# Kernel tuning notes

Measured on AMD Instinct MI355X. Metric: run time of the kernel, lower is better.

## Reference

```python
import jax, jax.numpy as jnp
import numpy as np

EPS = 1e-12  # F.normalize denominator clamp


def setup_inputs() -> dict:
    key = jax.random.key(0)
    k1, k2, k3, k4 = jax.random.split(key, 4)
    bs, d, nc, ncl, cs, ny = 8192, 768, 64, 500, 100, 1000
    train_embedding = jax.random.normal(k1, (bs, d), dtype=jnp.float32)
    clusters = jax.random.normal(k2, (ncl, cs, d), dtype=jnp.float32)
    # init_concept: uniform in [-0.5, 0.5]
    concept = jax.random.uniform(k3, (d, nc), dtype=jnp.float32, minval=-0.5, maxval=0.5)
    W_h = jax.random.normal(k4, (d, ny), dtype=jnp.float32) * 0.02
    b_h = jnp.zeros((ny,), dtype=jnp.float32)
    return {"train_embedding": train_embedding, "clusters": clusters,
            "concept": concept, "W_h": W_h, "b_h": b_h}


def reference(train_embedding, clusters, concept, W_h, b_h):
    # column-wise L2 normalize concept (F.normalize p=2 dim=0)
    concept_normalized = concept / jnp.maximum(
        jnp.linalg.norm(concept, axis=0, keepdims=True), EPS)
    # projection onto span(concept): C (C^T C)^-1 C^T
    gram = concept.T @ concept                      # [nc, nc]
    proj_matrix = concept @ jnp.linalg.inv(gram) @ concept.T  # [d, d]
    proj = proj_matrix @ train_embedding.T          # [d, bs]
    cluster_mean = jnp.mean(clusters, axis=1)       # [ncl, d]
    score_matrix = jnp.abs(cluster_mean @ concept_normalized)  # [ncl, nc]
    score_norm = score_matrix / jnp.maximum(
        jnp.linalg.norm(score_matrix, axis=0, keepdims=True), EPS)
    L_sparse_1 = jnp.sum(score_norm)
    # sum_{i != j} <score_norm[:,i], score_norm[:,j]> == sum(G) - trace(G)
    G = score_norm.T @ score_norm                   # [nc, nc]
    L_sparse_2 = jnp.sum(G) - jnp.trace(G)
    y_pred = proj.T @ W_h + b_h                     # h_x as linear head, [bs, ny]
    return (y_pred, L_sparse_1, L_sparse_2)
```

## Files before the change

kernel.cpp:

```cpp
#include <hip/hip_runtime.h>
#include <math.h>

#define BS   8192
#define DD   768
#define NC   64
#define NCL  500
#define CS   100
#define NY   1000
#define EPSN 1e-12f

#define NB_TMAT  256
#define NB_CMEAN 375
#define NB_GRAM  64
#define NB_U     32
#define NB_A     (NB_TMAT + NB_CMEAN + NB_GRAM + NB_U)

#define FMA4(acc, s, v) { (acc).x = fmaf((s), (v).x, (acc).x); \
                          (acc).y = fmaf((s), (v).y, (acc).y); \
                          (acc).z = fmaf((s), (v).z, (acc).z); \
                          (acc).w = fmaf((s), (v).w, (acc).w); }

__global__ __launch_bounds__(256) void k_phaseA(
    const float* __restrict__ clusters, const float* __restrict__ C,
    const float* __restrict__ W, const float* __restrict__ X,
    float* __restrict__ cm, float* __restrict__ gram,
    float* __restrict__ Up, float* __restrict__ Tp) {
    __shared__ __align__(16) char smem_raw[25600];
    int b   = blockIdx.x;
    int tid = threadIdx.x;

    if (b < NB_TMAT) {
        int tile = b >> 2, ks = b & 3;
        int r0g  = tile * 128, kb = ks * 192;
        float (*Xt)[132] = (float(*)[132])smem_raw;
        float (*Cs)[68]  = (float(*)[68])(smem_raw + 16896);
        int tx = tid & 15, ty = tid >> 4;
        float4 acc[8];
        #pragma unroll
        for (int r = 0; r < 8; ++r) acc[r] = make_float4(0.f, 0.f, 0.f, 0.f);
        for (int kc = kb; kc < kb + 192; kc += 32) {
            __syncthreads();
            {
                int row = tid & 127, kh = (tid >> 7) * 16;
                const float4* xp = (const float4*)(X + (size_t)(r0g + row) * DD + kc + kh);
                float4 x0 = xp[0], x1 = xp[1], x2 = xp[2], x3 = xp[3];
                Xt[kh+ 0][row]=x0.x; Xt[kh+ 1][row]=x0.y; Xt[kh+ 2][row]=x0.z; Xt[kh+ 3][row]=x0.w;
                Xt[kh+ 4][row]=x1.x; Xt[kh+ 5][row]=x1.y; Xt[kh+ 6][row]=x1.z; Xt[kh+ 7][row]=x1.w;
                Xt[kh+ 8][row]=x2.x; Xt[kh+ 9][row]=x2.y; Xt[kh+10][row]=x2.z; Xt[kh+11][row]=x2.w;
                Xt[kh+12][row]=x3.x; Xt[kh+13][row]=x3.y; Xt[kh+14][row]=x3.z; Xt[kh+15][row]=x3.w;
            }
            {
                int c4 = tid & 15, kk = tid >> 4;
                *((float4*)&Cs[kk][c4*4])      = *((const float4*)(C + (size_t)(kc+kk)*64 + c4*4));
                *((float4*)&Cs[kk+16][c4*4])   = *((const float4*)(C + (size_t)(kc+kk+16)*64 + c4*4));
            }
            __syncthreads();
            #pragma unroll 8
            for (int k = 0; k < 32; ++k) {
                float4 xa = *((float4*)&Xt[k][ty*8]);
                float4 xb = *((float4*)&Xt[k][ty*8+4]);
                float4 cb = *((float4*)&Cs[k][tx*4]);
                FMA4(acc[0], xa.x, cb); FMA4(acc[1], xa.y, cb);
                FMA4(acc[2], xa.z, cb); FMA4(acc[3], xa.w, cb);
                FMA4(acc[4], xb.x, cb); FMA4(acc[5], xb.y, cb);
                FMA4(acc[6], xb.z, cb); FMA4(acc[7], xb.w, cb);
            }
        }
        float* Tps = Tp + (size_t)ks * BS * 64;
        #pragma unroll
        for (int r = 0; r < 8; ++r)
            *((float4*)(Tps + (size_t)(r0g + ty*8 + r) * 64 + tx*4)) = acc[r];
    } else if (b < NB_TMAT + NB_CMEAN) {
        int idx = (b - NB_TMAT) * 256 + tid;
        int r  = idx / (DD / 4);
        int d4 = idx % (DD / 4);
        const float4* base = (const float4*)(clusters + (size_t)r * CS * DD) + d4;
        float4 a0 = {0,0,0,0}, a1 = {0,0,0,0}, a2 = {0,0,0,0}, a3 = {0,0,0,0};
        for (int s = 0; s < CS; s += 4) {
            float4 v0 = base[(size_t)(s + 0) * (DD / 4)];
            float4 v1 = base[(size_t)(s + 1) * (DD / 4)];
            float4 v2 = base[(size_t)(s + 2) * (DD / 4)];
            float4 v3 = base[(size_t)(s + 3) * (DD / 4)];
            a0.x += v0.x; a0.y += v0.y; a0.z += v0.z; a0.w += v0.w;
            a1.x += v1.x; a1.y += v1.y; a1.z += v1.z; a1.w += v1.w;
            a2.x += v2.x; a2.y += v2.y; a2.z += v2.z; a2.w += v2.w;
            a3.x += v3.x; a3.y += v3.y; a3.z += v3.z; a3.w += v3.w;
        }
        float4 o;
        const float sc = 1.0f / CS;
        o.x = (a0.x + a1.x + a2.x + a3.x) * sc;
        o.y = (a0.y + a1.y + a2.y + a3.y) * sc;
        o.z = (a0.z + a1.z + a2.z + a3.z) * sc;
        o.w = (a0.w + a1.w + a2.w + a3.w) * sc;
        ((float4*)cm)[idx] = o;
    } else if (b < NB_TMAT + NB_CMEAN + NB_GRAM) {
        int j   = b - (NB_TMAT + NB_CMEAN);
        int i   = tid & 63;
        int seg = tid >> 6;
        float p = 0.f;
        for (int k = seg * 192; k < seg * 192 + 192; ++k)
            p += C[k * NC + i] * C[k * NC + j];
        float (*red)[64] = (float(*)[64])smem_raw;
        red[seg][i] = p;
        __syncthreads();
        if (seg == 0)
            gram[i * NC + j] = red[0][i] + red[1][i] + red[2][i] + red[3][i];
    } else {
        int q  = b - (NB_TMAT + NB_CMEAN + NB_GRAM);
        int nt = q >> 2, ks = q & 3;
        int n0 = nt * 128, kb = ks * 192;
        float (*Cu)[68]  = (float(*)[68])smem_raw;
        float (*Wu)[132] = (float(*)[132])(smem_raw + 8704);
        int tx = tid & 15, ty = tid >> 4;
        float4 a0[4], a1[4];
        #pragma unroll
        for (int i = 0; i < 4; ++i) { a0[i] = make_float4(0,0,0,0); a1[i] = make_float4(0,0,0,0); }
        for (int kc = kb; kc < kb + 192; kc += 32) {
            __syncthreads();
            {   int i4 = tid & 15, kk = tid >> 4;
                *((float4*)&Cu[kk][i4*4])    = *((const float4*)(C + (size_t)(kc+kk)*64 + i4*4));
                *((float4*)&Cu[kk+16][i4*4]) = *((const float4*)(C + (size_t)(kc+kk+16)*64 + i4*4));
            }
            {   int nf = tid & 31, kq = tid >> 5;
                #pragma unroll
                for (int u = 0; u < 4; ++u) {
                    int k = kq + u * 8;
                    int n = n0 + nf * 4;
                    float4 v = {0.f, 0.f, 0.f, 0.f};
                    if (n < NY) v = *((const float4*)(W + (size_t)(kc + k) * NY + n));
                    *((float4*)&Wu[k][nf*4]) = v;
                }
            }
            __syncthreads();
            #pragma unroll 8
            for (int k = 0; k < 32; ++k) {
                float4 ci = *((float4*)&Cu[k][ty*4]);
                float4 w0 = *((float4*)&Wu[k][tx*8]);
                float4 w1 = *((float4*)&Wu[k][tx*8+4]);
                FMA4(a0[0], ci.x, w0); FMA4(a1[0], ci.x, w1);
                FMA4(a0[1], ci.y, w0); FMA4(a1[1], ci.y, w1);
                FMA4(a0[2], ci.z, w0); FMA4(a1[2], ci.z, w1);
                FMA4(a0[3], ci.w, w0); FMA4(a1[3], ci.w, w1);
            }
        }
        float* Ups = Up + (size_t)ks * 64000;
        #pragma unroll
        for (int i = 0; i < 4; ++i) {
            int irow = ty * 4 + i;
            int n = n0 + tx * 8;
            if (n < NY)     *((float4*)(Ups + (size_t)irow * NY + n))     = a0[i];
            if (n + 4 < NY) *((float4*)(Ups + (size_t)irow * NY + n + 4)) = a1[i];
        }
    }
}

__global__ __launch_bounds__(256) void k_phaseB(
    const float* __restrict__ gram, const float* __restrict__ cm,
    const float* __restrict__ C, float* __restrict__ ginv,
    float* __restrict__ SP) {
    __shared__ __align__(16) char smem_raw[25600];
    int blk = blockIdx.x;
    int tid = threadIdx.x;
    if (blk == 0) {
        int c = tid & 63;
        int q = tid >> 6;
        float a[16], bb[16];
        #pragma unroll
        for (int i = 0; i < 16; ++i) {
            int r = q * 16 + i;
            a[i]  = gram[r * 64 + c];
            bb[i] = (r == c) ? 1.f : 0.f;
        }
        __shared__ float asr[2][64];
        __shared__ float bsr[2][64];
        for (int p = 0; p < 64; ++p) {
            int qp  = p >> 4;
            int lp  = p & 15;
            int par = p & 1;
            if (q == qp) {
                float ap = 0.f, bp = 0.f;
                #pragma unroll
                for (int i = 0; i < 16; ++i)
                    if (i == lp) { ap = a[i]; bp = bb[i]; }
                float App = __shfl(ap, p);
                float s   = 1.0f / App;
                asr[par][c] = ap * s;
                bsr[par][c] = bp * s;
            }
            __syncthreads();
            float as_ = asr[par][c];
            float bs_ = bsr[par][c];
            #pragma unroll
            for (int i = 0; i < 16; ++i) {
                float f = __shfl(a[i], p);
                bool isp = (q == qp) && (i == lp);
                a[i]  = isp ? as_ : fmaf(-f, as_, a[i]);
                bb[i] = isp ? bs_ : fmaf(-f, bs_, bb[i]);
            }
        }
        #pragma unroll
        for (int i = 0; i < 16; ++i)
            ginv[(q * 16 + i) * 64 + c] = bb[i];
    } else {
        int q = blk - 1;
        int tile = q >> 2, ks = q & 3;
        int r0 = tile * 128, kb = ks * 192;
        float (*Mt)[132] = (float(*)[132])smem_raw;
        float (*Cs)[68]  = (float(*)[68])(smem_raw + 16896);
        int tx = tid & 15, ty = tid >> 4;
        float4 acc[8];
        #pragma unroll
        for (int r = 0; r < 8; ++r) acc[r] = make_float4(0.f, 0.f, 0.f, 0.f);
        for (int kc = kb; kc < kb + 192; kc += 32) {
            __syncthreads();
            {   int row = tid & 127, kh = (tid >> 7) * 16;
                int gr = r0 + row;
                int grc = gr < NCL ? gr : (NCL - 1);
                const float4* xp = (const float4*)(cm + (size_t)grc * DD + kc + kh);
                float4 x0 = xp[0], x1 = xp[1], x2 = xp[2], x3 = xp[3];
                Mt[kh+ 0][row]=x0.x; Mt[kh+ 1][row]=x0.y; Mt[kh+ 2][row]=x0.z; Mt[kh+ 3][row]=x0.w;
                Mt[kh+ 4][row]=x1.x; Mt[kh+ 5][row]=x1.y; Mt[kh+ 6][row]=x1.z; Mt[kh+ 7][row]=x1.w;
                Mt[kh+ 8][row]=x2.x; Mt[kh+ 9][row]=x2.y; Mt[kh+10][row]=x2.z; Mt[kh+11][row]=x2.w;
                Mt[kh+12][row]=x3.x; Mt[kh+13][row]=x3.y; Mt[kh+14][row]=x3.z; Mt[kh+15][row]=x3.w;
            }
            {   int c4 = tid & 15, kk = tid >> 4;
                *((float4*)&Cs[kk][c4*4])    = *((const float4*)(C + (size_t)(kc+kk)*64 + c4*4));
                *((float4*)&Cs[kk+16][c4*4]) = *((const float4*)(C + (size_t)(kc+kk+16)*64 + c4*4));
            }
            __syncthreads();
            #pragma unroll 8
            for (int k = 0; k < 32; ++k) {
                float4 xa = *((float4*)&Mt[k][ty*8]);
                float4 xb = *((float4*)&Mt[k][ty*8+4]);
                float4 cb = *((float4*)&Cs[k][tx*4]);
                FMA4(acc[0], xa.x, cb); FMA4(acc[1], xa.y, cb);
                FMA4(acc[2], xa.z, cb); FMA4(acc[3], xa.w, cb);
                FMA4(acc[4], xb.x, cb); FMA4(acc[5], xb.y, cb);
                FMA4(acc[6], xb.z, cb); FMA4(acc[7], xb.w, cb);
            }
        }
        float* SPs = SP + (size_t)ks * 32000;
        #pragma unroll
        for (int r = 0; r < 8; ++r) {
            int row = r0 + ty * 8 + r;
            if (row < NCL)
                *((float4*)(SPs + (size_t)row * 64 + tx*4)) = acc[r];
        }
    }
}

__global__ __launch_bounds__(256) void k_ypred(
    const float* __restrict__ Tp, const float* __restrict__ ginv,
    const float* __restrict__ Up, const float* __restrict__ bh,
    float* __restrict__ SP, float* __restrict__ Y,
    float* __restrict__ out2) {
    __shared__ __align__(16) char smem_raw[67584];
    int blk = blockIdx.x;
    int tid = threadIdx.x;
    if (blk == 1024) {
        __shared__ float colred[4][64];
        __shared__ float rn[64];
        __shared__ float trc[64];
        __shared__ float r1[4], r2[4];
        const float* SP0 = SP;
        const float* SP1 = SP + 32000;
        const float* SP2 = SP + 64000;
        const float* SP3 = SP + 96000;
        int c = tid & 63, seg = tid >> 6;
        float p = 0.f;
        for (int r = seg; r < NCL; r += 4) {
            int off = r * 64 + c;
            float s = fabsf(SP0[off] + SP1[off] + SP2[off] + SP3[off]);
            SP[off] = s;
            p += s * s;
        }
        colred[seg][c] = p;
        __syncthreads();
        if (seg == 0) {
            float n2  = colred[0][c] + colred[1][c] + colred[2][c] + colred[3][c];
            float inv = 1.0f / fmaxf(sqrtf(n2), EPSN);
            rn[c]  = inv;
            trc[c] = n2 * inv * inv;
        }
        __syncthreads();
        float l1p = 0.f, l2p = 0.f;
        for (int r = tid; r < NCL; r += 256) {
            float rs = 0.f;
            #pragma unroll
            for (int cc = 0; cc < 64; ++cc)
                rs += SP[r * 64 + cc] * rn[cc];
            l1p += rs;
            l2p += rs * rs;
        }
        #pragma unroll
        for (int off = 32; off > 0; off >>= 1) {
            l1p += __shfl_down(l1p, off);
            l2p += __shfl_down(l2p, off);
        }
        int wave = tid >> 6, lane = tid & 63;
        if (lane == 0) { r1[wave] = l1p; r2[wave] = l2p; }
        __syncthreads();
        if (tid == 0) {
            float L1 = r1[0] + r1[1] + r1[2] + r1[3];
            float L2 = r2[0] + r2[1] + r2[2] + r2[3];
            float tr = 0.f;
            #pragma unroll
            for (int cc = 0; cc < 64; ++cc) tr += trc[cc];
            out2[0] = L1;
            out2[1] = L2 - tr;
        }
        return;
    }
    float (*Ts)[132] = (float(*)[132])smem_raw;
    float (*Gs)[64]  = (float(*)[64])(smem_raw + 33792);
    float (*Vs)[68]  = (float(*)[68])(smem_raw + 50176);
    int rb = blk >> 4, cb = blk & 15;
    int r0g = rb * 128, c0g = cb * 64;
    const float* Tp0 = Tp;
    const float* Tp1 = Tp + (size_t)BS * 64;
    const float* Tp2 = Tp + (size_t)BS * 128;
    const float* Tp3 = Tp + (size_t)BS * 192;
    const float* Up0 = Up;
    const float* Up1 = Up + 64000;
    const float* Up2 = Up + 128000;
    const float* Up3 = Up + 192000;
    {
        int kf = tid & 15, rr = tid >> 4;
        #pragma unroll
        for (int p = 0; p < 8; ++p) {
            int row = rr + p * 16;
            size_t off = (size_t)(r0g + row) * 64 + kf * 4;
            float4 t0 = *((const float4*)(Tp0 + off));
            float4 t1 = *((const float4*)(Tp1 + off));
            float4 t2 = *((const float4*)(Tp2 + off));
            float4 t3 = *((const float4*)(Tp3 + off));
            float4 t;
            t.x = t0.x + t1.x + t2.x + t3.x;
            t.y = t0.y + t1.y + t2.y + t3.y;
            t.z = t0.z + t1.z + t2.z + t3.z;
            t.w = t0.w + t1.w + t2.w + t3.w;
            Ts[kf*4+0][row] = t.x; Ts[kf*4+1][row] = t.y;
            Ts[kf*4+2][row] = t.z; Ts[kf*4+3][row] = t.w;
        }
    }
    {
        #pragma unroll
        for (int p = 0; p < 4; ++p) {
            int f = tid + p * 256;
            int k = f >> 4, j4 = f & 15;
            *((float4*)&Gs[k][j4*4]) = *((const float4*)(ginv + k * 64 + j4*4));
        }
    }
    {
        #pragma unroll
        for (int p = 0; p < 4; ++p) {
            int f = tid + p * 256;
            int k = f >> 4, n4 = f & 15;
            int n = c0g + n4 * 4;
            float4 v = {0.f, 0.f, 0.f, 0.f};
            if (n < NY) {
                float4 u0 = *((const float4*)(Up0 + (size_t)k * NY + n));
                float4 u1 = *((const float4*)(Up1 + (size_t)k * NY + n));
                float4 u2 = *((const float4*)(Up2 + (size_t)k * NY + n));
                float4 u3 = *((const float4*)(Up3 + (size_t)k * NY + n));
                v.x = u0.x + u1.x + u2.x + u3.x;
                v.y = u0.y + u1.y + u2.y + u3.y;
                v.z = u0.z + u1.z + u2.z + u3.z;
                v.w = u0.w + u1.w + u2.w + u3.w;
            }
            *((float4*)&Vs[k][n4*4]) = v;
        }
    }
    __syncthreads();
    int tx = tid & 15, ty = tid >> 4;
    float4 tp[8];
    #pragma unroll
    for (int r = 0; r < 8; ++r) tp[r] = make_float4(0.f, 0.f, 0.f, 0.f);
    #pragma unroll 8
    for (int k = 0; k < 64; ++k) {
        float4 xa = *((float4*)&Ts[k][ty*8]);
        float4 xb = *((float4*)&Ts[k][ty*8+4]);
        float4 g  = *((float4*)&Gs[k][tx*4]);
        FMA4(tp[0], xa.x, g); FMA4(tp[1], xa.y, g);
        FMA4(tp[2], xa.z, g); FMA4(tp[3], xa.w, g);
        FMA4(tp[4], xb.x, g); FMA4(tp[5], xb.y, g);
        FMA4(tp[6], xb.z, g); FMA4(tp[7], xb.w, g);
    }
    __syncthreads();
    #pragma unroll
    for (int r = 0; r < 8; ++r) {
        int row = ty * 8 + r;
        Ts[tx*4+0][row] = tp[r].x;
        Ts[tx*4+1][row] = tp[r].y;
        Ts[tx*4+2][row] = tp[r].z;
        Ts[tx*4+3][row] = tp[r].w;
    }
    __syncthreads();
    int cx = tid & 15, ry = tid >> 4;
    float4 acc[8];
    #pragma unroll
    for (int r = 0; r < 8; ++r) acc[r] = make_float4(0.f, 0.f, 0.f, 0.f);
    #pragma unroll 8
    for (int k = 0; k < 64; ++k) {
        float4 xa = *((float4*)&Ts[k][ry*8]);
        float4 xb = *((float4*)&Ts[k][ry*8+4]);
        float4 v  = *((float4*)&Vs[k][cx*4]);
        FMA4(acc[0], xa.x, v); FMA4(acc[1], xa.y, v);
        FMA4(acc[2], xa.z, v); FMA4(acc[3], xa.w, v);
        FMA4(acc[4], xb.x, v); FMA4(acc[5], xb.y, v);
        FMA4(acc[6], xb.z, v); FMA4(acc[7], xb.w, v);
    }
    int col = c0g + cx * 4;
    if (col < NY) {
        float4 bias = *((const float4*)(bh + col));
        #pragma unroll
        for (int r = 0; r < 8; ++r) {
            int row = r0g + ry * 8 + r;
            float4 o;
            o.x = acc[r].x + bias.x;
            o.y = acc[r].y + bias.y;
            o.z = acc[r].z + bias.z;
            o.w = acc[r].w + bias.w;
            *((float4*)(Y + (size_t)row * NY + col)) = o;
        }
    }
}

extern "C" void kernel_launch(void* const* d_in, const int* in_sizes, int n_in,
                              void* d_out, int out_size, void* d_ws, size_t ws_size,
                              hipStream_t stream) {
    const float* X        = (const float*)d_in[0];
    const float* clusters = (const float*)d_in[1];
    const float* C        = (const float*)d_in[2];
    const float* W        = (const float*)d_in[3];
    const float* bh       = (const float*)d_in[4];
    float* out = (float*)d_out;
    float* ws  = (float*)d_ws;

    float* cm   = ws;
    float* gram = cm   + 384000;
    float* ginv = gram + 4096;
    float* Up   = ginv + 4096;
    float* SP   = Up   + 256000;
    float* Tp   = SP   + 128000;

    k_phaseA<<<dim3(NB_A), dim3(256), 0, stream>>>(clusters, C, W, X, cm, gram, Up, Tp);
    k_phaseB<<<dim3(17),   dim3(256), 0, stream>>>(gram, cm, C, ginv, SP);
    k_ypred <<<dim3(1025), dim3(256), 0, stream>>>(Tp, ginv, Up, bh, SP, out, out + (size_t)BS * NY);
}
```

Before: 174.2 us.

## Precompute ginv·U once and restructure GEMM tiles to row-major smem

Folds the ginv multiply into a small new kernel that computes V = ginv·U once, instead of every y_pred block redoing T·ginv. The final GEMM then becomes a single 64-deep T·V product using 128x128 output tiles. It also moves the cluster-mean reduction out of the fused phase-A kernel into its own launch, and switches the X/C and cm/C tiles to row-major shared-memory loads with 64-wide k chunks. The cost is two extra kernel launches and larger shared-memory footprints, which may lower occupancy.

Result: slower. 185.1 us (+6.3%).

```diff
diff --git a/kernel.cpp b/kernel.cpp
--- a/kernel.cpp
+++ b/kernel.cpp
@@ -9,92 +9,69 @@
 #define NY   1000
 #define EPSN 1e-12f
 
-#define NB_TMAT  256
-#define NB_CMEAN 375
-#define NB_GRAM  64
-#define NB_U     32
-#define NB_A     (NB_TMAT + NB_CMEAN + NB_GRAM + NB_U)
+#define NBT 256
+#define NBG 64
+#define NBU 32
 
 #define FMA4(acc, s, v) { (acc).x = fmaf((s), (v).x, (acc).x); \
                           (acc).y = fmaf((s), (v).y, (acc).y); \
                           (acc).z = fmaf((s), (v).z, (acc).z); \
                           (acc).w = fmaf((s), (v).w, (acc).w); }
 
-__global__ __launch_bounds__(256) void k_phaseA(
-    const float* __restrict__ clusters, const float* __restrict__ C,
-    const float* __restrict__ W, const float* __restrict__ X,
-    float* __restrict__ cm, float* __restrict__ gram,
+__global__ __launch_bounds__(256) void k_gemms(
+    const float* __restrict__ C, const float* __restrict__ W,
+    const float* __restrict__ X, float* __restrict__ gram,
     float* __restrict__ Up, float* __restrict__ Tp) {
-    __shared__ __align__(16) char smem_raw[25600];
-    int b   = blockIdx.x;
-    int tid = threadIdx.x;
-
-    if (b < NB_TMAT) {
+    __shared__ __align__(16) char smem_raw[52224];
+    int b = blockIdx.x, tid = threadIdx.x;
+
+    if (b < NBT) {
         int tile = b >> 2, ks = b & 3;
-        int r0g  = tile * 128, kb = ks * 192;
-        float (*Xt)[132] = (float(*)[132])smem_raw;
-        float (*Cs)[68]  = (float(*)[68])(smem_raw + 16896);
+        int r0 = tile * 128, kb = ks * 192;
+        float (*Xr)[68] = (float(*)[68])smem_raw;
+        float (*Cs)[68] = (float(*)[68])(smem_raw + 128*68*4);
         int tx = tid & 15, ty = tid >> 4;
         float4 acc[8];
         #pragma unroll
-        for (int r = 0; r < 8; ++r) acc[r] = make_float4(0.f, 0.f, 0.f, 0.f);
-        for (int kc = kb; kc < kb + 192; kc += 32) {
-            __syncthreads();
-            {
-                int row = tid & 127, kh = (tid >> 7) * 16;
-                const float4* xp = (const float4*)(X + (size_t)(r0g + row) * DD + kc + kh);
-                float4 x0 = xp[0], x1 = xp[1], x2 = xp[2], x3 = xp[3];
-                Xt[kh+ 0][row]=x0.x; Xt[kh+ 1][row]=x0.y; Xt[kh+ 2][row]=x0.z; Xt[kh+ 3][row]=x0.w;
-                Xt[kh+ 4][row]=x1.x; Xt[kh+ 5][row]=x1.y; Xt[kh+ 6][row]=x1.z; Xt[kh+ 7][row]=x1.w;
-                Xt[kh+ 8][row]=x2.x; Xt[kh+ 9][row]=x2.y; Xt[kh+10][row]=x2.z; Xt[kh+11][row]=x2.w;
-                Xt[kh+12][row]=x3.x; Xt[kh+13][row]=x3.y; Xt[kh+14][row]=x3.z; Xt[kh+15][row]=x3.w;
-            }
-            {
-                int c4 = tid & 15, kk = tid >> 4;
-                *((float4*)&Cs[kk][c4*4])      = *((const float4*)(C + (size_t)(kc+kk)*64 + c4*4));
-                *((float4*)&Cs[kk+16][c4*4])   = *((const float4*)(C + (size_t)(kc+kk+16)*64 + c4*4));
-            }
-            __syncthreads();
-            #pragma unroll 8
-            for (int k = 0; k < 32; ++k) {
-                float4 xa = *((float4*)&Xt[k][ty*8]);
-                float4 xb = *((float4*)&Xt[k][ty*8+4]);
-                float4 cb = *((float4*)&Cs[k][tx*4]);
-                FMA4(acc[0], xa.x, cb); FMA4(acc[1], xa.y, cb);
-                FMA4(acc[2], xa.z, cb); FMA4(acc[3], xa.w, cb);
-                FMA4(acc[4], xb.x, cb); FMA4(acc[5], xb.y, cb);
-                FMA4(acc[6], xb.z, cb); FMA4(acc[7], xb.w, cb);
+        for (int r = 0; r < 8; ++r) acc[r] = make_float4(0.f,0.f,0.f,0.f);
+        for (int kc = 0; kc < 192; kc += 64) {
+            __syncthreads();
+            #pragma unroll
+            for (int p = 0; p < 8; ++p) {
+                int f = tid + p * 256;
+                int row = f >> 4, k4 = f & 15;
+                *((float4*)&Xr[row][k4*4]) =
+                    *((const float4*)(X + (size_t)(r0+row)*DD + kb+kc + k4*4));
+            }
+            #pragma unroll
+            for (int p = 0; p < 4; ++p) {
+                int f = tid + p * 256;
+                int k = f >> 4, c4 = f & 15;
+                *((float4*)&Cs[k][c4*4]) =
+                    *((const float4*)(C + (size_t)(kb+kc+k)*64 + c4*4));
+            }
+            __syncthreads();
+            for (int k0 = 0; k0 < 64; k0 += 4) {
+                float4 cv0 = *((float4*)&Cs[k0+0][tx*4]);
+                float4 cv1 = *((float4*)&Cs[k0+1][tx*4]);
+                float4 cv2 = *((float4*)&Cs[k0+2][tx*4]);
+                float4 cv3 = *((float4*)&Cs[k0+3][tx*4]);
+                #pragma unroll
+                for (int r = 0; r < 8; ++r) {
+                    float4 xv = *((float4*)&Xr[ty*8+r][k0]);
+                    FMA4(acc[r], xv.x, cv0);
+                    FMA4(acc[r], xv.y, cv1);
+                    FMA4(acc[r], xv.z, cv2);
+                    FMA4(acc[r], xv.w, cv3);
+                }
             }
         }
         float* Tps = Tp + (size_t)ks * BS * 64;
         #pragma unroll
         for (int r = 0; r < 8; ++r)
-            *((float4*)(Tps + (size_t)(r0g + ty*8 + r) * 64 + tx*4)) = acc[r];
-    } else if (b < NB_TMAT + NB_CMEAN) {
-        int idx = (b - NB_TMAT) * 256 + tid;
-        int r  = idx / (DD / 4);
-        int d4 = idx % (DD / 4);
-        const float4* base = (const float4*)(clusters + (size_t)r * CS * DD) + d4;
-        float4 a0 = {0,0,0,0}, a1 = {0,0,0,0}, a2 = {0,0,0,0}, a3 = {0,0,0,0};
-        for (int s = 0; s < CS; s += 4) {
-            float4 v0 = base[(size_t)(s + 0) * (DD / 4)];
-            float4 v1 = base[(size_t)(s + 1) * (DD / 4)];
-            float4 v2 = base[(size_t)(s + 2) * (DD / 4)];
-            float4 v3 = base[(size_t)(s + 3) * (DD / 4)];
-            a0.x += v0.x; a0.y += v0.y; a0.z += v0.z; a0.w += v0.w;
-            a1.x += v1.x; a1.y += v1.y; a1.z += v1.z; a1.w += v1.w;
-            a2.x += v2.x; a2.y += v2.y; a2.z += v2.z; a2.w += v2.w;
-            a3.x += v3.x; a3.y += v3.y; a3.z += v3.z; a3.w += v3.w;
-        }
-        float4 o;
-        const float sc = 1.0f / CS;
-        o.x = (a0.x + a1.x + a2.x + a3.x) * sc;
-        o.y = (a0.y + a1.y + a2.y + a3.y) * sc;
-        o.z = (a0.z + a1.z + a2.z + a3.z) * sc;
-        o.w = (a0.w + a1.w + a2.w + a3.w) * sc;
-        ((float4*)cm)[idx] = o;
-    } else if (b < NB_TMAT + NB_CMEAN + NB_GRAM) {
-        int j   = b - (NB_TMAT + NB_CMEAN);
+            *((float4*)(Tps + (size_t)(r0 + ty*8 + r)*64 + tx*4)) = acc[r];
+    } else if (b < NBT + NBG) {
+        int j   = b - NBT;
         int i   = tid & 63;
         int seg = tid >> 6;
         float p = 0.f;
@@ -106,7 +83,7 @@
         if (seg == 0)
             gram[i * NC + j] = red[0][i] + red[1][i] + red[2][i] + red[3][i];
     } else {
-        int q  = b - (NB_TMAT + NB_CMEAN + NB_GRAM);
+        int q  = b - (NBT + NBG);
         int nt = q >> 2, ks = q & 3;
         int n0 = nt * 128, kb = ks * 192;
         float (*Cu)[68]  = (float(*)[68])smem_raw;
@@ -154,11 +131,37 @@
     }
 }
 
+__global__ __launch_bounds__(256) void k_cmean(const float* __restrict__ clusters,
+                                               float* __restrict__ cm) {
+    int idx = blockIdx.x * 256 + threadIdx.x;
+    int r  = idx / (DD / 4);
+    int d4 = idx % (DD / 4);
+    const float4* base = (const float4*)(clusters + (size_t)r * CS * DD) + d4;
+    float4 a0 = {0,0,0,0}, a1 = {0,0,0,0}, a2 = {0,0,0,0}, a3 = {0,0,0,0};
+    for (int s = 0; s < CS; s += 4) {
+        float4 v0 = base[(size_t)(s + 0) * (DD / 4)];
+        float4 v1 = base[(size_t)(s + 1) * (DD / 4)];
+        float4 v2 = base[(size_t)(s + 2) * (DD / 4)];
+        float4 v3 = base[(size_t)(s + 3) * (DD / 4)];
+        a0.x += v0.x; a0.y += v0.y; a0.z += v0.z; a0.w += v0.w;
+        a1.x += v1.x; a1.y += v1.y; a1.z += v1.z; a1.w += v1.w;
+        a2.x += v2.x; a2.y += v2.y; a2.z += v2.z; a2.w += v2.w;
+        a3.x += v3.x; a3.y += v3.y; a3.z += v3.z; a3.w += v3.w;
+    }
+    float4 o;
+    const float sc = 1.0f / CS;
+    o.x = (a0.x + a1.x + a2.x + a3.x) * sc;
+    o.y = (a0.y + a1.y + a2.y + a3.y) * sc;
+    o.z = (a0.z + a1.z + a2.z + a3.z) * sc;
+    o.w = (a0.w + a1.w + a2.w + a3.w) * sc;
+    ((float4*)cm)[idx] = o;
+}
+
 __global__ __launch_bounds__(256) void k_phaseB(
     const float* __restrict__ gram, const float* __restrict__ cm,
     const float* __restrict__ C, float* __restrict__ ginv,
     float* __restrict__ SP) {
-    __shared__ __align__(16) char smem_raw[25600];
+    __shared__ __align__(16) char smem_raw[52224];
     int blk = blockIdx.x;
     int tid = threadIdx.x;
     if (blk == 0) {
@@ -205,38 +208,44 @@
         int q = blk - 1;
         int tile = q >> 2, ks = q & 3;
         int r0 = tile * 128, kb = ks * 192;
-        float (*Mt)[132] = (float(*)[132])smem_raw;
-        float (*Cs)[68]  = (float(*)[68])(smem_raw + 16896);
+        float (*Mr)[68] = (float(*)[68])smem_raw;
+        float (*Cs)[68] = (float(*)[68])(smem_raw + 128*68*4);
         int tx = tid & 15, ty = tid >> 4;
         float4 acc[8];
         #pragma unroll
-        for (int r = 0; r < 8; ++r) acc[r] = make_float4(0.f, 0.f, 0.f, 0.f);
-        for (int kc = kb; kc < kb + 192; kc += 32) {
-            __syncthreads();
-            {   int row = tid & 127, kh = (tid >> 7) * 16;
+        for (int r = 0; r < 8; ++r) acc[r] = make_float4(0.f,0.f,0.f,0.f);
+        for (int kc = 0; kc < 192; kc += 64) {
+            __syncthreads();
+            #pragma unroll
+            for (int p = 0; p < 8; ++p) {
+                int f = tid + p * 256;
+                int row = f >> 4, k4 = f & 15;
                 int gr = r0 + row;
                 int grc = gr < NCL ? gr : (NCL - 1);
-                const float4* xp = (const float4*)(cm + (size_t)grc * DD + kc + kh);
-                float4 x0 = xp[0], x1 = xp[1], x2 = xp[2], x3 = xp[3];
-                Mt[kh+ 0][row]=x0.x; Mt[kh+ 1][row]=x0.y; Mt[kh+ 2][row]=x0.z; Mt[kh+ 3][row]=x0.w;
-                Mt[kh+ 4][row]=x1.x; Mt[kh+ 5][row]=x1.y; Mt[kh+ 6][row]=x1.z; Mt[kh+ 7][row]=x1.w;
-                Mt[kh+ 8][row]=x2.x; Mt[kh+ 9][row]=x2.y; Mt[kh+10][row]=x2.z; Mt[kh+11][row]=x2.w;
-                Mt[kh+12][row]=x3.x; Mt[kh+13][row]=x3.y; Mt[kh+14][row]=x3.z; Mt[kh+15][row]=x3.w;
-            }
-            {   int c4 = tid & 15, kk = tid >> 4;
-                *((float4*)&Cs[kk][c4*4])    = *((const float4*)(C + (size_t)(kc+kk)*64 + c4*4));
-                *((float4*)&Cs[kk+16][c4*4]) = *((const float4*)(C + (size_t)(kc+kk+16)*64 + c4*4));
-            }
-            __syncthreads();
-            #pragma unroll 8
-            for (int k = 0; k < 32; ++k) {
-                float4 xa = *((float4*)&Mt[k][ty*8]);
-                float4 xb = *((float4*)&Mt[k][ty*8+4]);
-                float4 cb = *((float4*)&Cs[k][tx*4]);
-                FMA4(acc[0], xa.x, cb); FMA4(acc[1], xa.y, cb);
-                FMA4(acc[2], xa.z, cb); FMA4(acc[3], xa.w, cb);
-                FMA4(acc[4], xb.x, cb); FMA4(acc[5], xb.y, cb);
-                FMA4(acc[6], xb.z, cb); FMA4(acc[7], xb.w, cb);
+                *((float4*)&Mr[row][k4*4]) =
+                    *((const float4*)(cm + (size_t)grc*DD + kb+kc + k4*4));
+            }
+            #pragma unroll
+            for (int p = 0; p < 4; ++p) {
+                int f = tid + p * 256;
+                int k = f >> 4, c4 = f & 15;
+                *((float4*)&Cs[k][c4*4]) =
+                    *((const float4*)(C + (size_t)(kb+kc+k)*64 + c4*4));
+            }
+            __syncthreads();
+            for (int k0 = 0; k0 < 64; k0 += 4) {
+                float4 cv0 = *((float4*)&Cs[k0+0][tx*4]);
+                float4 cv1 = *((float4*)&Cs[k0+1][tx*4]);
+                float4 cv2 = *((float4*)&Cs[k0+2][tx*4]);
+                float4 cv3 = *((float4*)&Cs[k0+3][tx*4]);
+                #pragma unroll
+                for (int r = 0; r < 8; ++r) {
+                    float4 xv = *((float4*)&Mr[ty*8+r][k0]);
+                    FMA4(acc[r], xv.x, cv0);
+                    FMA4(acc[r], xv.y, cv1);
+                    FMA4(acc[r], xv.z, cv2);
+                    FMA4(acc[r], xv.w, cv3);
+                }
             }
         }
         float* SPs = SP + (size_t)ks * 32000;
@@ -249,15 +258,12 @@
     }
 }
 
-__global__ __launch_bounds__(256) void k_ypred(
-    const float* __restrict__ Tp, const float* __restrict__ ginv,
-    const float* __restrict__ Up, const float* __restrict__ bh,
-    float* __restrict__ SP, float* __restrict__ Y,
-    float* __restrict__ out2) {
-    __shared__ __align__(16) char smem_raw[67584];
-    int blk = blockIdx.x;
-    int tid = threadIdx.x;
-    if (blk == 1024) {
+__global__ __launch_bounds__(256) void k_vc(
+    const float* __restrict__ ginv, const float* __restrict__ Up,
+    float* __restrict__ SP, float* __restrict__ V, float* __restrict__ out2) {
+    __shared__ __align__(16) char smem_raw[34816];
+    int blk = blockIdx.x, tid = threadIdx.x;
+    if (blk == 16) {
         __shared__ float colred[4][64];
         __shared__ float rn[64];
         __shared__ float trc[64];
@@ -311,117 +317,131 @@
         }
         return;
     }
-    float (*Ts)[132] = (float(*)[132])smem_raw;
-    float (*Gs)[64]  = (float(*)[64])(smem_raw + 33792);
-    float (*Vs)[68]  = (float(*)[68])(smem_raw + 50176);
-    int rb = blk >> 4, cb = blk & 15;
-    int r0g = rb * 128, c0g = cb * 64;
+    float (*Us)[68] = (float(*)[68])smem_raw;
+    float (*Gs)[68] = (float(*)[68])(smem_raw + 64*68*4);
+    int c0 = blk * 64;
+    int tx = tid & 15, ty = tid >> 4;
+    const float* Up0 = Up;
+    const float* Up1 = Up + 64000;
+    const float* Up2 = Up + 128000;
+    const float* Up3 = Up + 192000;
+    #pragma unroll
+    for (int p = 0; p < 4; ++p) {
+        int f = tid + p * 256;
+        int j = f >> 4, n4 = f & 15;
+        int n = c0 + n4 * 4;
+        float4 v = {0.f, 0.f, 0.f, 0.f};
+        if (n < NY) {
+            float4 u0 = *((const float4*)(Up0 + (size_t)j * NY + n));
+            float4 u1 = *((const float4*)(Up1 + (size_t)j * NY + n));
+            float4 u2 = *((const float4*)(Up2 + (size_t)j * NY + n));
+            float4 u3 = *((const float4*)(Up3 + (size_t)j * NY + n));
+            v.x = u0.x + u1.x + u2.x + u3.x;
+            v.y = u0.y + u1.y + u2.y + u3.y;
+            v.z = u0.z + u1.z + u2.z + u3.z;
+            v.w = u0.w + u1.w + u2.w + u3.w;
+        }
+        *((float4*)&Us[j][n4*4]) = v;
+        *((float4*)&Gs[j][n4*4]) = *((const float4*)(ginv + (size_t)j * 64 + n4*4));
+    }
+    __syncthreads();
+    float4 acc[4];
+    #pragma unroll
+    for (int i = 0; i < 4; ++i) acc[i] = make_float4(0.f,0.f,0.f,0.f);
+    for (int j0 = 0; j0 < 64; j0 += 4) {
+        #pragma unroll
+        for (int jj = 0; jj < 4; ++jj) {
+            float4 g = *((float4*)&Gs[j0+jj][ty*4]);
+            float4 u = *((float4*)&Us[j0+jj][tx*4]);
+            FMA4(acc[0], g.x, u);
+            FMA4(acc[1], g.y, u);
+            FMA4(acc[2], g.z, u);
+            FMA4(acc[3], g.w, u);
+        }
+    }
+    #pragma unroll
+    for (int i = 0; i < 4; ++i) {
+        int n = c0 + tx * 4;
+        if (n < NY)
+            *((float4*)(V + (size_t)(ty*4 + i) * NY + n)) = acc[i];
+    }
+}
+
+__global__ __launch_bounds__(256) void k_ypred(
+    const float* __restrict__ Tp, const float* __restrict__ V,
+    const float* __restrict__ bh, float* __restrict__ Y) {
+    __shared__ __align__(16) char smem_raw[68608];
+    float (*Tr)[68]  = (float(*)[68])smem_raw;
+    float (*Vs)[132] = (float(*)[132])(smem_raw + 128*68*4);
+    int blk = blockIdx.x, tid = threadIdx.x;
+    int rb = blk >> 3, cb = blk & 7;
+    int r0g = rb * 128, c0g = cb * 128;
     const float* Tp0 = Tp;
     const float* Tp1 = Tp + (size_t)BS * 64;
     const float* Tp2 = Tp + (size_t)BS * 128;
     const float* Tp3 = Tp + (size_t)BS * 192;
-    const float* Up0 = Up;
-    const float* Up1 = Up + 64000;
-    const float* Up2 = Up + 128000;
-    const float* Up3 = Up + 192000;
-    {
-        int kf = tid & 15, rr = tid >> 4;
-        #pragma unroll
-        for (int p = 0; p < 8; ++p) {
-            int row = rr + p * 16;
-            size_t off = (size_t)(r0g + row) * 64 + kf * 4;
-            float4 t0 = *((const float4*)(Tp0 + off));
-            float4 t1 = *((const float4*)(Tp1 + off));
-            float4 t2 = *((const float4*)(Tp2 + off));
-            float4 t3 = *((const float4*)(Tp3 + off));
-            float4 t;
-            t.x = t0.x + t1.x + t2.x + t3.x;
-            t.y = t0.y + t1.y + t2.y + t3.y;
-            t.z = t0.z + t1.z + t2.z + t3.z;
-            t.w = t0.w + t1.w + t2.w + t3.w;
-            Ts[kf*4+0][row] = t.x; Ts[kf*4+1][row] = t.y;
-            Ts[kf*4+2][row] = t.z; Ts[kf*4+3][row] = t.w;
-        }
-    }
-    {
-        #pragma unroll
-        for (int p = 0; p < 4; ++p) {
-            int f = tid + p * 256;
-            int k = f >> 4, j4 = f & 15;
-            *((float4*)&Gs[k][j4*4]) = *((const float4*)(ginv + k * 64 + j4*4));
-        }
-    }
-    {
-        #pragma unroll
-        for (int p = 0; p < 4; ++p) {
-            int f = tid + p * 256;
-            int k = f >> 4, n4 = f & 15;
-            int n = c0g + n4 * 4;
-            float4 v = {0.f, 0.f, 0.f, 0.f};
-            if (n < NY) {
-                float4 u0 = *((const float4*)(Up0 + (size_t)k * NY + n));
-                float4 u1 = *((const float4*)(Up1 + (size_t)k * NY + n));
-                float4 u2 = *((const float4*)(Up2 + (size_t)k * NY + n));
-                float4 u3 = *((const float4*)(Up3 + (size_t)k * NY + n));
-                v.x = u0.x + u1.x + u2.x + u3.x;
-                v.y = u0.y + u1.y + u2.y + u3.y;
-                v.z = u0.z + u1.z + u2.z + u3.z;
-                v.w = u0.w + u1.w + u2.w + u3.w;
-            }
-            *((float4*)&Vs[k][n4*4]) = v;
-        }
-    }
-    __syncthreads();
-    int tx = tid & 15, ty = tid >> 4;
-    float4 tp[8];
-    #pragma unroll
-    for (int r = 0; r < 8; ++r) tp[r] = make_float4(0.f, 0.f, 0.f, 0.f);
-    #pragma unroll 8
-    for (int k = 0; k < 64; ++k) {
-        float4 xa = *((float4*)&Ts[k][ty*8]);
-        float4 xb = *((float4*)&Ts[k][ty*8+4]);
-        float4 g  = *((float4*)&Gs[k][tx*4]);
-        FMA4(tp[0], xa.x, g); FMA4(tp[1], xa.y, g);
-        FMA4(tp[2], xa.z, g); FMA4(tp[3], xa.w, g);
-        FMA4(tp[4], xb.x, g); FMA4(tp[5], xb.y, g);
-        FMA4(tp[6], xb.z, g); FMA4(tp[7], xb.w, g);
-    }
-    __syncthreads();
-    #pragma unroll
-    for (int r = 0; r < 8; ++r) {
-        int row = ty * 8 + r;
-        Ts[tx*4+0][row] = tp[r].x;
-        Ts[tx*4+1][row] = tp[r].y;
-        Ts[tx*4+2][row] = tp[r].z;
-        Ts[tx*4+3][row] = tp[r].w;
+    #pragma unroll
+    for (int p = 0; p < 8; ++p) {
+        int f = tid + p * 256;
+        int row = f >> 4, k4 = f & 15;
+        size_t off = (size_t)(r0g + row) * 64 + k4 * 4;
+        float4 t0 = *((const float4*)(Tp0 + off));
+        float4 t1 = *((const float4*)(Tp1 + off));
+        float4 t2 = *((const float4*)(Tp2 + off));
+        float4 t3 = *((const float4*)(Tp3 + off));
+        float4 t;
+        t.x = t0.x + t1.x + t2.x + t3.x;
+        t.y = t0.y + t1.y + t2.y + t3.y;
+        t.z = t0.z + t1.z + t2.z + t3.z;
+        t.w = t0.w + t1.w + t2.w + t3.w;
+        *((float4*)&Tr[row][k4*4]) = t;
+    }
+    #pragma unroll
+    for (int p = 0; p < 8; ++p) {
+        int f = tid + p * 256;
+        int k = f >> 5, n8 = f & 31;
+        int n = c0g + n8 * 4;
+        float4 v = {0.f, 0.f, 0.f, 0.f};
+        if (n < NY) v = *((const float4*)(V + (size_t)k * NY + n));
+        *((float4*)&Vs[k][n8*4]) = v;
     }
     __syncthreads();
     int cx = tid & 15, ry = tid >> 4;
-    float4 acc[8];
-    #pragma unroll
-    for (int r = 0; r < 8; ++r) acc[r] = make_float4(0.f, 0.f, 0.f, 0.f);
-    #pragma unroll 8
-    for (int k = 0; k < 64; ++k) {
-        float4 xa = *((float4*)&Ts[k][ry*8]);
-        float4 xb = *((float4*)&Ts[k][ry*8+4]);
-        float4 v  = *((float4*)&Vs[k][cx*4]);
-        FMA4(acc[0], xa.x, v); FMA4(acc[1], xa.y, v);
-        FMA4(acc[2], xa.z, v); FMA4(acc[3], xa.w, v);
-        FMA4(acc[4], xb.x, v); FMA4(acc[5], xb.y, v);
-        FMA4(acc[6], xb.z, v); FMA4(acc[7], xb.w, v);
-    }
-    int col = c0g + cx * 4;
-    if (col < NY) {
-        float4 bias = *((const float4*)(bh + col));
+    float4 lo[8], hi[8];
+    #pragma unroll
+    for (int r = 0; r < 8; ++r) { lo[r] = make_float4(0.f,0.f,0.f,0.f); hi[r] = lo[r]; }
+    for (int k0 = 0; k0 < 64; k0 += 4) {
+        float4 va0 = *((float4*)&Vs[k0+0][cx*8]), vb0 = *((float4*)&Vs[k0+0][cx*8+4]);
+        float4 va1 = *((float4*)&Vs[k0+1][cx*8]), vb1 = *((float4*)&Vs[k0+1][cx*8+4]);
+        float4 va2 = *((float4*)&Vs[k0+2][cx*8]), vb2 = *((float4*)&Vs[k0+2][cx*8+4]);
+        float4 va3 = *((float4*)&Vs[k0+3][cx*8]), vb3 = *((float4*)&Vs[k0+3][cx*8+4]);
         #pragma unroll
         for (int r = 0; r < 8; ++r) {
-            int row = r0g + ry * 8 + r;
+            float4 tv = *((float4*)&Tr[ry*8+r][k0]);
+            FMA4(lo[r], tv.x, va0); FMA4(hi[r], tv.x, vb0);
+            FMA4(lo[r], tv.y, va1); FMA4(hi[r], tv.y, vb1);
+            FMA4(lo[r], tv.z, va2); FMA4(hi[r], tv.z, vb2);
+            FMA4(lo[r], tv.w, va3); FMA4(hi[r], tv.w, vb3);
+        }
+    }
+    int cbase = c0g + cx * 8;
+    float4 bias0 = {0,0,0,0}, bias1 = {0,0,0,0};
+    if (cbase < NY)     bias0 = *((const float4*)(bh + cbase));
+    if (cbase + 4 < NY) bias1 = *((const float4*)(bh + cbase + 4));
+    #pragma unroll
+    for (int r = 0; r < 8; ++r) {
+        int row = r0g + ry * 8 + r;
+        if (cbase < NY) {
             float4 o;
-            o.x = acc[r].x + bias.x;
-            o.y = acc[r].y + bias.y;
-            o.z = acc[r].z + bias.z;
-            o.w = acc[r].w + bias.w;
-            *((float4*)(Y + (size_t)row * NY + col)) = o;
+            o.x = lo[r].x + bias0.x; o.y = lo[r].y + bias0.y;
+            o.z = lo[r].z + bias0.z; o.w = lo[r].w + bias0.w;
+            *((float4*)(Y + (size_t)row * NY + cbase)) = o;
+        }
+        if (cbase + 4 < NY) {
+            float4 o;
+            o.x = hi[r].x + bias1.x; o.y = hi[r].y + bias1.y;
+            o.z = hi[r].z + bias1.z; o.w = hi[r].w + bias1.w;
+            *((float4*)(Y + (size_t)row * NY + cbase + 4)) = o;
         }
     }
 }
@@ -442,9 +462,12 @@
     float* ginv = gram + 4096;
     float* Up   = ginv + 4096;
     float* SP   = Up   + 256000;
-    float* Tp   = SP   + 128000;
-
-    k_phaseA<<<dim3(NB_A), dim3(256), 0, stream>>>(clusters, C, W, X, cm, gram, Up, Tp);
-    k_phaseB<<<dim3(17),   dim3(256), 0, stream>>>(gram, cm, C, ginv, SP);
-    k_ypred <<<dim3(1025), dim3(256), 0, stream>>>(Tp, ginv, Up, bh, SP, out, out + (size_t)BS * NY);
-}
+    float* V    = SP   + 128000;
+    float* Tp   = V    + 64000;
+
+    k_gemms <<<dim3(NBT + NBG + NBU), dim3(256), 0, stream>>>(C, W, X, gram, Up, Tp);
+    k_cmean <<<dim3(375), dim3(256), 0, stream>>>(clusters, cm);
+    k_phaseB<<<dim3(17),  dim3(256), 0, stream>>>(gram, cm, C, ginv, SP);
+    k_vc    <<<dim3(17),  dim3(256), 0, stream>>>(ginv, Up, SP, V, out + (size_t)BS * NY);
+    k_ypred <<<dim3(512), dim3(256), 0, stream>>>(Tp, V, bh, out);
+}
```
